# Performance work log

Hardware: AMD Instinct MI355X
Metric: run time of the kernel (lower is better)

The kernel has to match this reference:

```python
import jax, jax.numpy as jnp
import numpy as np

NUM_CLASSES = 2
KS = 5  # kernel_size
EPS = 1e-8  # torch cosine_similarity eps


def setup_inputs() -> dict:
    key = jax.random.key(0)
    k1, k2, k3 = jax.random.split(key, 3)
    b, c, h, w = 8, 256, 128, 128
    er_input = jax.random.normal(k1, (b, c, h, w), dtype=jnp.float32)
    seg_label = jax.random.randint(k2, (b, h, w), 0, 2, dtype=jnp.int32)
    gt_boundary_seg = jax.random.randint(k3, (b, h, w), 0, 2, dtype=jnp.int32)
    return {"er_input": er_input, "seg_label": seg_label, "gt_boundary_seg": gt_boundary_seg}


def _context_loss(er_input, seg_label, gt_boundary_seg):
    # seg_label / gt_boundary_seg already at er_input spatial size (nearest interp is identity)
    b, c, h, w = er_input.shape
    r = KS // 2
    seg0 = jnp.where(seg_label == 255, 0, seg_label)
    gtb0 = jnp.where(gt_boundary_seg == 255, 0, gt_boundary_seg)
    gt_b = gtb0 * seg0                                  # [b,h,w] boundary pixels on fg classes
    interior = jnp.zeros((h, w), bool).at[r:h - r, r:w - r].set(True)
    valid = (gt_b > 0) & interior                       # pixels whose 5x5 window is in-bounds
    include = (gt_b > 0).any(axis=(1, 2))               # images contributing to scale_num
    cnt = valid.sum(axis=(1, 2)).astype(er_input.dtype)  # [b]

    norm = jnp.maximum(jnp.sqrt((er_input * er_input).sum(axis=1)), EPS)  # [b,h,w]
    validf = valid.astype(er_input.dtype)
    total = jnp.zeros((b,), dtype=er_input.dtype)
    n_shift = 0
    for dy in range(-r, r + 1):
        for dx in range(-r, r + 1):
            if dy == 0 and dx == 0:
                continue
            n_shift += 1
            # value at p+ (dy,dx) brought to p; valid pixels are interior so no wrap issue
            feat_s = jnp.roll(er_input, (-dy, -dx), axis=(2, 3))
            norm_s = jnp.roll(norm, (-dy, -dx), axis=(1, 2))
            seg_s = jnp.roll(seg_label, (-dy, -dx), axis=(1, 2))
            dot = (er_input * feat_s).sum(axis=1)       # [b,h,w]
            cos = dot / (norm * norm_s)
            # one_hot(seg,256)[:num_classes] dot product == labels equal AND label < num_classes
            labsim = ((seg_label == seg_s) & (seg_label < NUM_CLASSES)).astype(er_input.dtype)
            sq = (cos - labsim) ** 2
            # mse_loss over selected boundary pixels of image i
            total = total + (sq * validf).sum(axis=(1, 2)) / jnp.maximum(cnt, 1.0)
    loss_i = total / float(n_shift)                     # per-image context_loss_pi / 24
    scale_num = jnp.maximum(include.sum(), 1)
    return (loss_i * include.astype(loss_i.dtype)).sum() / scale_num.astype(loss_i.dtype)


def reference(er_input, seg_label, gt_boundary_seg):
    return _context_loss(er_input, seg_label, gt_boundary_seg)
```

## Files before the change

kernel.cpp:

```cpp
#include <hip/hip_runtime.h>
#include <math.h>

#define BATCH 8
#define CH    256
#define H     128
#define W     128
#define PLANE (H * W)
#define NPIX  (BATCH * PLANE)
#define NSHIFT 12
#define NCHUNK 4
#define CPC    (CH / NCHUNK)

static __device__ __constant__ int S_DY[NSHIFT] = {0,0,1,1,1,1,1,2,2,2,2,2};
static __device__ __constant__ int S_DX[NSHIFT] = {1,2,-2,-1,0,1,2,-2,-1,0,1,2};

#define NZERO4 ((13 * NPIX + 16) / 4)
#define NZB    ((NZERO4 + 255) / 256)

#define NCORRB (BATCH * 32 * NCHUNK)
#define NSTATB (BATCH * 64)

__device__ __forceinline__ void fma4(float& acc, const float4& a, const float4& b) {
    acc = fmaf(a.x, b.x, acc);
    acc = fmaf(a.y, b.y, acc);
    acc = fmaf(a.z, b.z, acc);
    acc = fmaf(a.w, b.w, acc);
}

__global__ __launch_bounds__(256) void k_prep(float4* __restrict__ p,
                                              float* __restrict__ out) {
    int i = blockIdx.x * 256 + threadIdx.x;
    if (i < NZERO4) p[i] = make_float4(0.f, 0.f, 0.f, 0.f);
    if (i == 0) out[0] = 0.0f;
}

__global__ __launch_bounds__(256) void k_corr(const float* __restrict__ er,
                                              const int* __restrict__ seg,
                                              const int* __restrict__ gtb,
                                              float* __restrict__ dots,
                                              float* __restrict__ normsq,
                                              int* __restrict__ cnt,
                                              int* __restrict__ inc) {
    __shared__ float4 lds[6][132];
    int t = threadIdx.x;

    if (blockIdx.x >= NCORRB) {
        int blk2 = blockIdx.x - NCORRB;
        int b = blk2 >> 6;
        int i = (blk2 & 63) * 256 + t;
        int my_cnt = 0, my_any = 0;
        {
            int s = seg[b * PLANE + i];
            int g = gtb[b * PLANE + i];
            int s0 = (s == 255) ? 0 : s;
            int g0 = (g == 255) ? 0 : g;
            if (s0 > 0 && g0 > 0) {
                my_any = 1;
                int y = i >> 7, x = i & 127;
                if (y >= 2 && y < H - 2 && x >= 2 && x < W - 2) my_cnt = 1;
            }
        }
        for (int o = 32; o > 0; o >>= 1) {
            my_cnt += __shfl_down(my_cnt, o, 64);
            my_any |= __shfl_down(my_any, o, 64);
        }
        __shared__ int sc[4], sa[4];
        int lane = t & 63, wid = t >> 6;
        if (lane == 0) { sc[wid] = my_cnt; sa[wid] = my_any; }
        __syncthreads();
        if (t == 0) {
            int c = sc[0] + sc[1] + sc[2] + sc[3];
            int a = sa[0] | sa[1] | sa[2] | sa[3];
            if (c) atomicAdd(&cnt[b], c);
            if (a) atomicOr(&inc[b], 1);
        }
        return;
    }

    int blk = blockIdx.x;
    int chunk = blk & 3;
    int tile  = (blk >> 2) & 31;
    int b     = blk >> 7;
    int y0 = tile * 4;
    int c0 = chunk * CPC;
    int r = t >> 7;
    int x = t & 127;

    if (t < 24) {
        int row = t >> 2, col = t & 3;
        int xs = (col < 2) ? col : (col + 128);
        lds[row][xs] = make_float4(0.f, 0.f, 0.f, 0.f);
    }

    float accA[13], accB[13];
#pragma unroll
    for (int i = 0; i < 13; i++) { accA[i] = 0.0f; accB[i] = 0.0f; }

    const float* base = er + (size_t)b * CH * PLANE;

    for (int c = c0; c < c0 + CPC; c += 4) {
        __syncthreads();
#pragma unroll
        for (int k = 0; k < 3; ++k) {
            int s = t + k * 256;
            int row = s >> 7;
            int xs = s & 127;
            int y = y0 + row;
            float4 v = make_float4(0.f, 0.f, 0.f, 0.f);
            if (y < H) {
                const float* p0 = base + (size_t)c * PLANE + y * W + xs;
                v.x = p0[0];
                v.y = p0[PLANE];
                v.z = p0[2 * PLANE];
                v.w = p0[3 * PLANE];
            }
            lds[row][xs + 2] = v;
        }
        __syncthreads();

        const float4* lp = &lds[2 * r][x + 2];
        float4 cA = lp[0];
        float4 cB = lp[132];
        {
            float4 v1 = lp[1], v2 = lp[2];
            fma4(accA[0], cA, cA);
            fma4(accA[1], cA, v1);
            fma4(accA[2], cA, v2);
        }
        {
            float4 m2 = lp[130], m1 = lp[131], p1 = lp[133], p2 = lp[134];
            fma4(accA[3], cA, m2);
            fma4(accA[4], cA, m1);
            fma4(accA[5], cA, cB);
            fma4(accA[6], cA, p1);
            fma4(accA[7], cA, p2);
            fma4(accB[0], cB, cB);
            fma4(accB[1], cB, p1);
            fma4(accB[2], cB, p2);
        }
        {
            float4 m2 = lp[262], m1 = lp[263], v0 = lp[264], p1 = lp[265], p2 = lp[266];
            fma4(accA[8],  cA, m2);
            fma4(accA[9],  cA, m1);
            fma4(accA[10], cA, v0);
            fma4(accA[11], cA, p1);
            fma4(accA[12], cA, p2);
            fma4(accB[3], cB, m2);
            fma4(accB[4], cB, m1);
            fma4(accB[5], cB, v0);
            fma4(accB[6], cB, p1);
            fma4(accB[7], cB, p2);
        }
        {
            float4 m2 = lp[394], m1 = lp[395], v0 = lp[396], p1 = lp[397], p2 = lp[398];
            fma4(accB[8],  cB, m2);
            fma4(accB[9],  cB, m1);
            fma4(accB[10], cB, v0);
            fma4(accB[11], cB, p1);
            fma4(accB[12], cB, p2);
        }
    }

    int pixA = b * PLANE + (y0 + 2 * r) * W + x;
    int pixB = pixA + W;
    atomicAdd(&normsq[pixA], accA[0]);
    atomicAdd(&normsq[pixB], accB[0]);
#pragma unroll
    for (int i = 0; i < NSHIFT; ++i) {
        atomicAdd(&dots[i * NPIX + pixA], accA[i + 1]);
        atomicAdd(&dots[i * NPIX + pixB], accB[i + 1]);
    }
}

__global__ __launch_bounds__(256) void k_loss(const float* __restrict__ dots,
                                              const float* __restrict__ normsq,
                                              const int* __restrict__ seg,
                                              const int* __restrict__ gtb,
                                              const int* __restrict__ cnt,
                                              const int* __restrict__ inc,
                                              float* __restrict__ out) {
    int idx = blockIdx.x * 256 + threadIdx.x;
    int b = idx >> 14;
    int rem = idx & (PLANE - 1);
    int y = rem >> 7;
    int x = rem & 127;

    int sn = 0;
#pragma unroll
    for (int b2 = 0; b2 < BATCH; b2++) sn += (inc[b2] != 0);
    if (sn < 1) sn = 1;
    int cb = cnt[b]; if (cb < 1) cb = 1;
    float factor = inc[b] ? 1.0f / (24.0f * (float)cb * (float)sn) : 0.0f;

    float val = 0.0f;
    if (y >= 2 && y < H - 2 && x >= 2 && x < W - 2) {
        int sp = seg[idx];
        int gp = gtb[idx];
        int s0 = (sp == 255) ? 0 : sp;
        int g0 = (gp == 255) ? 0 : gp;
        if (s0 > 0 && g0 > 0) {
            float np = fmaxf(sqrtf(normsq[idx]), 1e-8f);
            float sum = 0.0f;
#pragma unroll
            for (int i = 0; i < NSHIFT; ++i) {
                int off = S_DY[i] * W + S_DX[i];
                {
                    float d  = dots[i * NPIX + idx];
                    float nn = fmaxf(sqrtf(normsq[idx + off]), 1e-8f);
                    float cosv = d / (np * nn);
                    int sq = seg[idx + off];
                    float lab = (sp == sq && sp < 2) ? 1.0f : 0.0f;
                    float tt = cosv - lab;
                    sum = fmaf(tt, tt, sum);
                }
                {
                    float d  = dots[i * NPIX + idx - off];
                    float nn = fmaxf(sqrtf(normsq[idx - off]), 1e-8f);
                    float cosv = d / (np * nn);
                    int sq = seg[idx - off];
                    float lab = (sp == sq && sp < 2) ? 1.0f : 0.0f;
                    float tt = cosv - lab;
                    sum = fmaf(tt, tt, sum);
                }
            }
            val = sum * factor;
        }
    }

    for (int o = 32; o > 0; o >>= 1)
        val += __shfl_down(val, o, 64);
    __shared__ float wsum[4];
    int lane = threadIdx.x & 63;
    int wid  = threadIdx.x >> 6;
    if (lane == 0) wsum[wid] = val;
    __syncthreads();
    if (threadIdx.x == 0) {
        float s = wsum[0] + wsum[1] + wsum[2] + wsum[3];
        atomicAdd(out, s);
    }
}

extern "C" void kernel_launch(void* const* d_in, const int* in_sizes, int n_in,
                              void* d_out, int out_size, void* d_ws, size_t ws_size,
                              hipStream_t stream) {
    const float* er  = (const float*)d_in[0];
    const int*   seg = (const int*)d_in[1];
    const int*   gtb = (const int*)d_in[2];
    float* out = (float*)d_out;

    float* ws     = (float*)d_ws;
    float* dots   = ws;
    float* normsq = dots + NSHIFT * NPIX;
    int*   cnt    = (int*)(normsq + NPIX);
    int*   inc    = cnt + 8;

    hipLaunchKernelGGL(k_prep, dim3(NZB), dim3(256), 0, stream, (float4*)d_ws, out);
    hipLaunchKernelGGL(k_corr, dim3(NCORRB + NSTATB), dim3(256), 0, stream,
                       er, seg, gtb, dots, normsq, cnt, inc);
    hipLaunchKernelGGL(k_loss, dim3(NPIX / 256), dim3(256), 0, stream,
                       dots, normsq, seg, gtb, cnt, inc, out);
}
```

Baseline: 230.4 us.

## Replace atomic accumulation with per-chunk slices, register prefetch, and combine pass

Each channel chunk now writes its partial dot products and norms to its own slice with plain stores instead of float atomics, and a new combine kernel sums the slices. This removes the large workspace zeroing pass. The channel split doubles to 8 chunks for more blocks, and the next channel quad is prefetched into registers while the current one is computed from LDS. The cost is much more workspace traffic: 8 slices of 13 maps are written and read back, on top of an extra kernel launch.

```diff
diff --git a/kernel.cpp b/kernel.cpp
--- a/kernel.cpp
+++ b/kernel.cpp
@@ -8,14 +8,13 @@
 #define PLANE (H * W)
 #define NPIX  (BATCH * PLANE)
 #define NSHIFT 12
-#define NCHUNK 4
+#define NMAPS  13
+#define NCHUNK 8
 #define CPC    (CH / NCHUNK)
+#define SLICE  (NMAPS * NPIX)
 
 static __device__ __constant__ int S_DY[NSHIFT] = {0,0,1,1,1,1,1,2,2,2,2,2};
 static __device__ __constant__ int S_DX[NSHIFT] = {1,2,-2,-1,0,1,2,-2,-1,0,1,2};
-
-#define NZERO4 ((13 * NPIX + 16) / 4)
-#define NZB    ((NZERO4 + 255) / 256)
 
 #define NCORRB (BATCH * 32 * NCHUNK)
 #define NSTATB (BATCH * 64)
@@ -27,18 +26,17 @@
     acc = fmaf(a.w, b.w, acc);
 }
 
-__global__ __launch_bounds__(256) void k_prep(float4* __restrict__ p,
-                                              float* __restrict__ out) {
-    int i = blockIdx.x * 256 + threadIdx.x;
-    if (i < NZERO4) p[i] = make_float4(0.f, 0.f, 0.f, 0.f);
-    if (i == 0) out[0] = 0.0f;
+__global__ void k_prep(int* __restrict__ cnt, int* __restrict__ inc,
+                       float* __restrict__ out) {
+    int t = threadIdx.x;
+    if (t < 8) { cnt[t] = 0; inc[t] = 0; }
+    if (t == 0) out[0] = 0.0f;
 }
 
 __global__ __launch_bounds__(256) void k_corr(const float* __restrict__ er,
                                               const int* __restrict__ seg,
                                               const int* __restrict__ gtb,
-                                              float* __restrict__ dots,
-                                              float* __restrict__ normsq,
+                                              float* __restrict__ slices,
                                               int* __restrict__ cnt,
                                               int* __restrict__ inc) {
     __shared__ float4 lds[6][132];
@@ -78,9 +76,9 @@
     }
 
     int blk = blockIdx.x;
-    int chunk = blk & 3;
-    int tile  = (blk >> 2) & 31;
-    int b     = blk >> 7;
+    int chunk = blk & 7;
+    int tile  = (blk >> 3) & 31;
+    int b     = blk >> 8;
     int y0 = tile * 4;
     int c0 = chunk * CPC;
     int r = t >> 7;
@@ -98,25 +96,39 @@
 
     const float* base = er + (size_t)b * CH * PLANE;
 
-    for (int c = c0; c < c0 + CPC; c += 4) {
-        __syncthreads();
+    float pf[3][4];
+    auto load_quad = [&](int c) {
 #pragma unroll
         for (int k = 0; k < 3; ++k) {
             int s = t + k * 256;
             int row = s >> 7;
             int xs = s & 127;
             int y = y0 + row;
-            float4 v = make_float4(0.f, 0.f, 0.f, 0.f);
             if (y < H) {
                 const float* p0 = base + (size_t)c * PLANE + y * W + xs;
-                v.x = p0[0];
-                v.y = p0[PLANE];
-                v.z = p0[2 * PLANE];
-                v.w = p0[3 * PLANE];
+                pf[k][0] = p0[0];
+                pf[k][1] = p0[PLANE];
+                pf[k][2] = p0[2 * PLANE];
+                pf[k][3] = p0[3 * PLANE];
+            } else {
+                pf[k][0] = 0.f; pf[k][1] = 0.f; pf[k][2] = 0.f; pf[k][3] = 0.f;
             }
-            lds[row][xs + 2] = v;
-        }
+        }
+    };
+
+    load_quad(c0);
+    const int iters = CPC / 4;
+    for (int it = 0; it < iters; ++it) {
         __syncthreads();
+#pragma unroll
+        for (int k = 0; k < 3; ++k) {
+            int s = t + k * 256;
+            int row = s >> 7;
+            int xs = s & 127;
+            lds[row][xs + 2] = make_float4(pf[k][0], pf[k][1], pf[k][2], pf[k][3]);
+        }
+        __syncthreads();
+        if (it + 1 < iters) load_quad(c0 + 4 * (it + 1));
 
         const float4* lp = &lds[2 * r][x + 2];
         float4 cA = lp[0];
@@ -161,24 +173,38 @@
         }
     }
 
+    float* sp = slices + (size_t)chunk * SLICE;
     int pixA = b * PLANE + (y0 + 2 * r) * W + x;
     int pixB = pixA + W;
-    atomicAdd(&normsq[pixA], accA[0]);
-    atomicAdd(&normsq[pixB], accB[0]);
-#pragma unroll
-    for (int i = 0; i < NSHIFT; ++i) {
-        atomicAdd(&dots[i * NPIX + pixA], accA[i + 1]);
-        atomicAdd(&dots[i * NPIX + pixB], accB[i + 1]);
-    }
-}
-
-__global__ __launch_bounds__(256) void k_loss(const float* __restrict__ dots,
-                                              const float* __restrict__ normsq,
+#pragma unroll
+    for (int m = 0; m < NSHIFT; ++m) {
+        sp[m * NPIX + pixA] = accA[m + 1];
+        sp[m * NPIX + pixB] = accB[m + 1];
+    }
+    sp[NSHIFT * NPIX + pixA] = accA[0];
+    sp[NSHIFT * NPIX + pixB] = accB[0];
+}
+
+__global__ __launch_bounds__(256) void k_combine(const float4* __restrict__ sl,
+                                                 float4* __restrict__ comb) {
+    int i = blockIdx.x * 256 + threadIdx.x;
+    float4 s = sl[i];
+#pragma unroll
+    for (int c = 1; c < NCHUNK; ++c) {
+        float4 v = sl[(size_t)c * (SLICE / 4) + i];
+        s.x += v.x; s.y += v.y; s.z += v.z; s.w += v.w;
+    }
+    comb[i] = s;
+}
+
+__global__ __launch_bounds__(256) void k_loss(const float* __restrict__ comb,
                                               const int* __restrict__ seg,
                                               const int* __restrict__ gtb,
                                               const int* __restrict__ cnt,
                                               const int* __restrict__ inc,
                                               float* __restrict__ out) {
+    const float* dots   = comb;
+    const float* normsq = comb + NSHIFT * NPIX;
     int idx = blockIdx.x * 256 + threadIdx.x;
     int b = idx >> 14;
     int rem = idx & (PLANE - 1);
@@ -249,14 +275,16 @@
     float* out = (float*)d_out;
 
     float* ws     = (float*)d_ws;
-    float* dots   = ws;
-    float* normsq = dots + NSHIFT * NPIX;
-    int*   cnt    = (int*)(normsq + NPIX);
+    float* comb   = ws;
+    float* slices = comb + SLICE;
+    int*   cnt    = (int*)(slices + (size_t)NCHUNK * SLICE);
     int*   inc    = cnt + 8;
 
-    hipLaunchKernelGGL(k_prep, dim3(NZB), dim3(256), 0, stream, (float4*)d_ws, out);
-    hipLaunchKernelGGL(k_corr, dim3(NCORRB + NSTATB), dim3(256), 0, stream,
-                       er, seg, gtb, dots, normsq, cnt, inc);
-    hipLaunchKernelGGL(k_loss, dim3(NPIX / 256), dim3(256), 0, stream,
-                       dots, normsq, seg, gtb, cnt, inc, out);
-}
+    hipLaunchKernelGGL(k_prep,    dim3(1), dim3(64), 0, stream, cnt, inc, out);
+    hipLaunchKernelGGL(k_corr,    dim3(NCORRB + NSTATB), dim3(256), 0, stream,
+                       er, seg, gtb, slices, cnt, inc);
+    hipLaunchKernelGGL(k_combine, dim3(SLICE / 4 / 256), dim3(256), 0, stream,
+                       (const float4*)slices, (float4*)comb);
+    hipLaunchKernelGGL(k_loss,    dim3(NPIX / 256), dim3(256), 0, stream,
+                       comb, seg, gtb, cnt, inc, out);
+}
```

New measurement: 221.9 us. 1.04x faster.
